# Optimization experiments

Measured on AMD Instinct MI355X. Metric: run time of the kernel, lower is better.

## Reference

```python
import jax, jax.numpy as jnp
import numpy as np

C, CP, H, D, N, B = 128, 16, 8, 16, 2048, 1
INF = 1e8


def _ln(x, w=None, b=None, eps=1e-5):
    mu = jnp.mean(x, axis=-1, keepdims=True)
    var = jnp.var(x, axis=-1, keepdims=True)
    y = (x - mu) * jax.lax.rsqrt(var + eps)
    if w is not None:
        y = y * w
    if b is not None:
        y = y + b
    return y


def _ada_ln(a, s, sln_w, gw, gb, skw):
    # AdaLN: non-affine LN on a, weight-only LN on s, sigmoid gate + skip from s
    a = _ln(a)
    s = _ln(s, sln_w)
    return jax.nn.sigmoid(s @ gw + gb) * a + s @ skw


def _betas(n, n_keys=128, inf=INF):
    # centers at 16 + 32k; query row i belongs to window i//32, keys within +/- n_keys//2 of center
    i = jnp.arange(n)
    c = 16 + 32 * (i // 32)
    j = jnp.arange(n)
    ok = (j[None, :] >= (c - n_keys // 2)[:, None]) & (j[None, :] < (c + n_keys // 2)[:, None])
    return jnp.where(ok, 0.0, -inf).astype(jnp.float32)


def _forward(atom_single, atom_proj, atom_pair, mask,
             a_sln_w, a_gate_w, a_gate_b, a_skip_w,
             wq, bq, wk, wv, wg, bg, wo, bo,
             lnz_w, lnz_b, wz, wog, bog,
             t_sln_w, t_gate_w, t_gate_b, t_skip_w,
             w_sw, w_hid, w_out, t_wog, t_bog):
    bs, n, _ = atom_single.shape
    betas = _betas(n)
    # ---- AttentionPairBias (input_gating=True, residual handled outside) ----
    a = _ada_ln(atom_single, atom_proj, a_sln_w, a_gate_w, a_gate_b, a_skip_w)
    q = (a @ wq + bq).reshape(bs, n, H, D)
    k = (a @ wk).reshape(bs, n, H, D)
    v = (a @ wv).reshape(bs, n, H, D)
    pair_bias = _ln(atom_pair, lnz_w, lnz_b) @ wz            # (bs, n, n, H)
    pair_bias = jnp.transpose(pair_bias, (0, 3, 1, 2)) + betas  # (bs, H, n, n)
    mask_bias = (INF * (mask - 1.0))[:, None, None, :]          # (bs, 1, 1, n)
    logits = jnp.einsum('bqhd,bkhd->bhqk', q, k) / np.float32(np.sqrt(D))
    logits = logits + pair_bias + mask_bias
    probs = jax.nn.softmax(logits, axis=-1)
    o = jnp.einsum('bhqk,bkhd->bqhd', probs, v)
    g = jax.nn.sigmoid(a @ wg + bg).reshape(bs, n, H, D)
    o = (o * g).reshape(bs, n, H * D) @ wo + bo
    o = jax.nn.sigmoid(atom_proj @ wog + bog) * o             # conditioned output gate
    atom_single = atom_single + o
    # ---- ConditionedTransitionBlock (SwiGLU, n=2) ----
    t = _ada_ln(atom_single, atom_proj, t_sln_w, t_gate_w, t_gate_b, t_skip_w)
    hidden = jax.nn.silu(t @ w_sw) * (t @ w_hid)              # (bs, n, 2C)
    t_out = jax.nn.sigmoid(atom_proj @ t_wog + t_bog) * (hidden @ w_out)
    return atom_single + t_out


def setup_inputs() -> dict:
    key = jax.random.key(0)
    ks = iter(jax.random.split(key, 40))
    rn = lambda shape, s=1.0: jax.random.normal(next(ks), shape, jnp.float32) * s
    p = 0.05
    return {
        "atom_single": rn((B, N, C)),
        "atom_proj": rn((B, N, C)),
        "atom_pair": rn((B, N, N, CP)),
        "mask": jnp.ones((B, N), jnp.float32),
        "a_sln_w": jnp.ones((C,), jnp.float32), "a_gate_w": rn((C, C), p), "a_gate_b": jnp.zeros((C,), jnp.float32), "a_skip_w": rn((C, C), p),
        "wq": rn((C, C), p), "bq": jnp.zeros((C,), jnp.float32),
        "wk": rn((C, C), p), "wv": rn((C, C), p),
        "wg": rn((C, C), p), "bg": jnp.ones((C,), jnp.float32),
        "wo": rn((C, C), p), "bo": jnp.zeros((C,), jnp.float32),
        "lnz_w": jnp.ones((CP,), jnp.float32), "lnz_b": jnp.zeros((CP,), jnp.float32), "wz": rn((CP, H), p),
        "wog": rn((C, C), p), "bog": jnp.full((C,), -2.0, jnp.float32),
        "t_sln_w": jnp.ones((C,), jnp.float32), "t_gate_w": rn((C, C), p), "t_gate_b": jnp.zeros((C,), jnp.float32), "t_skip_w": rn((C, C), p),
        "w_sw": rn((C, 2 * C), p), "w_hid": rn((C, 2 * C), p), "w_out": rn((2 * C, C), p),
        "t_wog": rn((C, C), p), "t_bog": jnp.full((C,), -2.0, jnp.float32),
    }


def reference(atom_single, atom_proj, atom_pair, mask,
              a_sln_w, a_gate_w, a_gate_b, a_skip_w,
              wq, bq, wk, wv, wg, bg, wo, bo,
              lnz_w, lnz_b, wz, wog, bog,
              t_sln_w, t_gate_w, t_gate_b, t_skip_w,
              w_sw, w_hid, w_out, t_wog, t_bog):
    out = _forward(atom_single, atom_proj, atom_pair, mask,
                   a_sln_w, a_gate_w, a_gate_b, a_skip_w,
                   wq, bq, wk, wv, wg, bg, wo, bo,
                   lnz_w, lnz_b, wz, wog, bog,
                   t_sln_w, t_gate_w, t_gate_b, t_skip_w,
                   w_sw, w_hid, w_out, t_wog, t_bog)
    return (out, atom_proj, atom_pair)
```

## Files before the change

kernel.cpp:

```cpp
#include <hip/hip_runtime.h>
#include <math.h>

#define NN 2048
#define CC 128
#define HH 8
#define DD 16
#define NKEY 128
#define INFV 1e8f
#define NPR ((long)NN * CC / 4)
#define NCPTOT (NPR + (long)NN * NN * 4)
#define SLOT 2176
#define ANP 36
#define ASLOT 1152

typedef float f4 __attribute__((ext_vector_type(4)));

__device__ __forceinline__ float sigm(float x) { return 1.f / (1.f + expf(-x)); }

struct Args {
  const float *atom_single, *atom_proj, *atom_pair, *mask;
  const float *a_sln_w, *a_gate_w, *a_gate_b, *a_skip_w;
  const float *wq, *bq, *wk, *wv, *wg, *bg, *wo, *bo;
  const float *lnz_w, *lnz_b, *wz, *wog, *bog;
  const float *t_sln_w, *t_gate_w, *t_gate_b, *t_skip_w;
  const float *w_sw, *w_hid, *w_out, *t_wog, *t_bog;
  float *out;
  float *s_ln_t, *a_mat, *qm, *km, *vm, *gm, *ogm, *single2, *t_mat, *hidden, *bias;
  long cut[8];
};

__device__ __forceinline__ void copy_span(const Args& a, int s, long rb, long nb, int tid) {
  long c0 = a.cut[s], c1 = a.cut[s + 1];
  const f4* proj4 = (const f4*)a.atom_proj;
  const f4* pair4 = (const f4*)a.atom_pair;
  f4* dst = (f4*)(a.out + (long)NN * CC);
  long stride = nb * 256;
  long i = c0 + rb * 256 + tid;
  for (; i + 3 * stride < c1; i += 4 * stride) {
    long i1 = i + stride, i2 = i + 2 * stride, i3 = i + 3 * stride;
    f4 x0 = (i  < NPR) ? __builtin_nontemporal_load(&proj4[i])
                       : __builtin_nontemporal_load(&pair4[i - NPR]);
    f4 x1 = (i1 < NPR) ? __builtin_nontemporal_load(&proj4[i1])
                       : __builtin_nontemporal_load(&pair4[i1 - NPR]);
    f4 x2 = (i2 < NPR) ? __builtin_nontemporal_load(&proj4[i2])
                       : __builtin_nontemporal_load(&pair4[i2 - NPR]);
    f4 x3 = (i3 < NPR) ? __builtin_nontemporal_load(&proj4[i3])
                       : __builtin_nontemporal_load(&pair4[i3 - NPR]);
    __builtin_nontemporal_store(x0, &dst[i]);
    __builtin_nontemporal_store(x1, &dst[i1]);
    __builtin_nontemporal_store(x2, &dst[i2]);
    __builtin_nontemporal_store(x3, &dst[i3]);
  }
  for (; i < c1; i += stride) {
    f4 v = (i < NPR) ? __builtin_nontemporal_load(&proj4[i])
                     : __builtin_nontemporal_load(&pair4[i - NPR]);
    __builtin_nontemporal_store(v, &dst[i]);
  }
}

__device__ __forceinline__ void gsingle_pf(float* sm, int tid,
    const float* __restrict__ A1, const float* __restrict__ B1, int lda1, int ldb1, int K1,
    int r0, int c0, float acc1[4][4]) {
  float* buf0 = sm;
  float* buf1 = sm + 2 * SLOT;
  int tr = (tid >> 4) * 4, tc = (tid & 15) * 4;
  int ar = tid >> 5, ak = tid & 31;
  int bk = tid >> 6, bc = tid & 63;
  float pA[2][8], pB[2][8];
  auto LD = [&](int kb, int s) {
#pragma unroll
    for (int j = 0; j < 8; ++j) {
      pA[s][j] = A1[(long)(r0 + ar + 8 * j) * lda1 + kb + ak];
      pB[s][j] = B1[(long)(kb + bk + 4 * j) * ldb1 + c0 + bc];
    }
  };
  auto WR = [&](float* buf, int s) {
    float* B1s_ = buf + SLOT;
#pragma unroll
    for (int j = 0; j < 8; ++j) {
      buf[ak * 68 + ar + 8 * j] = pA[s][j];
      B1s_[(bk + 4 * j) * 68 + bc] = pB[s][j];
    }
  };
  auto CMP = [&](float* cur) {
    float* As_ = cur;
    float* B1s_ = cur + SLOT;
#pragma unroll 4
    for (int k = 0; k < 32; ++k) {
      float4 a1 = *(const float4*)&As_[k * 68 + tr];
      float4 b1 = *(const float4*)&B1s_[k * 68 + tc];
      float a1v[4] = {a1.x, a1.y, a1.z, a1.w};
      float b1v[4] = {b1.x, b1.y, b1.z, b1.w};
#pragma unroll
      for (int i = 0; i < 4; ++i)
#pragma unroll
        for (int j = 0; j < 4; ++j) acc1[i][j] = fmaf(a1v[i], b1v[j], acc1[i][j]);
    }
  };
  int nk = K1 / 32;
  LD(0, 0);
  if (nk > 1) LD(32, 1);
  WR(buf0, 0);
  __syncthreads();
  for (int kt = 0; kt < nk; kt += 2) {
    if (kt + 2 < nk) LD((kt + 2) * 32, 0);
    if (kt + 1 < nk) WR(buf1, 1);
    CMP(buf0);
    __syncthreads();
    if (kt + 1 >= nk) break;
    if (kt + 3 < nk) LD((kt + 3) * 32, 1);
    if (kt + 2 < nk) WR(buf0, 0);
    CMP(buf1);
    __syncthreads();
  }
}

template <bool SHA>
__device__ __forceinline__ void gdual32(float* sm, int tid,
    const float* __restrict__ A1, const float* __restrict__ B1, int lda1, int ldb1, int K1,
    const float* __restrict__ A2, const float* __restrict__ B2, int lda2, int ldb2, int K2,
    int r0, int c0, float acc1[2][4], float acc2[2][4]) {
  const int offB1 = ASLOT;
  const int offA2 = ASLOT + SLOT;
  const int offB2 = SHA ? (ASLOT + SLOT) : (2 * ASLOT + SLOT);
  const int bufsz = SHA ? (ASLOT + 2 * SLOT) : (2 * ASLOT + 2 * SLOT);
  float* buf0 = sm;
  float* buf1 = sm + bufsz;
  int tr2 = (tid >> 4) * 2, tc4 = (tid & 15) * 4;
  int ar = tid & 31, ak4 = (tid >> 5) * 4;
  int bk = tid >> 6, bc = tid & 63;
  float4 vA1[2], vA2[2];
  float pB1[2][8], pB2[2][8];

  auto LD = [&](int kb, int s, bool twof) {
    vA1[s] = *(const float4*)&A1[(long)(r0 + ar) * lda1 + kb + ak4];
#pragma unroll
    for (int j = 0; j < 8; ++j)
      pB1[s][j] = B1[(long)(kb + bk + 4 * j) * ldb1 + c0 + bc];
    if (twof) {
      if constexpr (!SHA) vA2[s] = *(const float4*)&A2[(long)(r0 + ar) * lda2 + kb + ak4];
#pragma unroll
      for (int j = 0; j < 8; ++j)
        pB2[s][j] = B2[(long)(kb + bk + 4 * j) * ldb2 + c0 + bc];
    }
  };
  auto WR = [&](float* buf, int s, bool twof) {
    float* As_ = buf;
    float* B1s_ = buf + offB1;
    As_[(ak4 + 0) * ANP + ar] = vA1[s].x;
    As_[(ak4 + 1) * ANP + ar] = vA1[s].y;
    As_[(ak4 + 2) * ANP + ar] = vA1[s].z;
    As_[(ak4 + 3) * ANP + ar] = vA1[s].w;
#pragma unroll
    for (int j = 0; j < 8; ++j) B1s_[(bk + 4 * j) * 68 + bc] = pB1[s][j];
    if (twof) {
      float* B2s_ = buf + offB2;
      if constexpr (!SHA) {
        float* A2s_ = buf + offA2;
        A2s_[(ak4 + 0) * ANP + ar] = vA2[s].x;
        A2s_[(ak4 + 1) * ANP + ar] = vA2[s].y;
        A2s_[(ak4 + 2) * ANP + ar] = vA2[s].z;
        A2s_[(ak4 + 3) * ANP + ar] = vA2[s].w;
      }
#pragma unroll
      for (int j = 0; j < 8; ++j) B2s_[(bk + 4 * j) * 68 + bc] = pB2[s][j];
    }
  };
  auto CMP = [&](float* cur, bool twoc) {
    float* As_ = cur;
    float* B1s_ = cur + offB1;
    float* A2s_ = cur + offA2;
    float* B2s_ = cur + offB2;
    if (twoc) {
#pragma unroll 4
      for (int k = 0; k < 32; ++k) {
        float2 a1 = *(const float2*)&As_[k * ANP + tr2];
        float4 b1 = *(const float4*)&B1s_[k * 68 + tc4];
        float4 b2 = *(const float4*)&B2s_[k * 68 + tc4];
        float2 a2;
        if constexpr (SHA) a2 = a1; else a2 = *(const float2*)&A2s_[k * ANP + tr2];
        float a1v[2] = {a1.x, a1.y};
        float a2v[2] = {a2.x, a2.y};
        float b1v[4] = {b1.x, b1.y, b1.z, b1.w};
        float b2v[4] = {b2.x, b2.y, b2.z, b2.w};
#pragma unroll
        for (int i = 0; i < 2; ++i)
#pragma unroll
          for (int j = 0; j < 4; ++j) {
            acc1[i][j] = fmaf(a1v[i], b1v[j], acc1[i][j]);
            acc2[i][j] = fmaf(a2v[i], b2v[j], acc2[i][j]);
          }
      }
    } else {
#pragma unroll 4
      for (int k = 0; k < 32; ++k) {
        float2 a1 = *(const float2*)&As_[k * ANP + tr2];
        float4 b1 = *(const float4*)&B1s_[k * 68 + tc4];
        float a1v[2] = {a1.x, a1.y};
        float b1v[4] = {b1.x, b1.y, b1.z, b1.w};
#pragma unroll
        for (int i = 0; i < 2; ++i)
#pragma unroll
          for (int j = 0; j < 4; ++j) acc1[i][j] = fmaf(a1v[i], b1v[j], acc1[i][j]);
      }
    }
  };

  int nk = K1 / 32;
  LD(0, 0, 0 < K2);
  if (nk > 1) LD(32, 1, 32 < K2);
  WR(buf0, 0, 0 < K2);
  __syncthreads();
  for (int kt = 0; kt < nk; kt += 2) {
    if (kt + 2 < nk) LD((kt + 2) * 32, 0, (kt + 2) * 32 < K2);
    if (kt + 1 < nk) WR(buf1, 1, (kt + 1) * 32 < K2);
    CMP(buf0, kt * 32 < K2);
    __syncthreads();
    if (kt + 1 >= nk) break;
    if (kt + 3 < nk) LD((kt + 3) * 32, 1, (kt + 3) * 32 < K2);
    if (kt + 2 < nk) WR(buf0, 0, (kt + 2) * 32 < K2);
    CMP(buf1, (kt + 1) * 32 < K2);
    __syncthreads();
  }
}

__device__ __forceinline__ void gdual32_ln(float* sm, int tid,
    const float* __restrict__ proj, const float* __restrict__ w_ln,
    const float* __restrict__ B1, const float* __restrict__ B2,
    int r0, int c0, const float* sst, float acc1[2][4], float acc2[2][4]) {
  const int offB1 = ASLOT;
  const int offB2 = ASLOT + SLOT;
  const int bufsz = ASLOT + 2 * SLOT;
  float* buf0 = sm;
  float* buf1 = sm + bufsz;
  int tr2 = (tid >> 4) * 2, tc4 = (tid & 15) * 4;
  int ar = tid & 31, ak4 = (tid >> 5) * 4;
  int bk = tid >> 6, bc = tid & 63;
  float4 vA1[2];
  float pB1[2][8], pB2[2][8];

  auto LD = [&](int kb, int s) {
    float4 raw = *(const float4*)&proj[(long)(r0 + ar) * CC + kb + ak4];
    float4 wv = *(const float4*)&w_ln[kb + ak4];
    float mu = sst[2 * ar], rs = sst[2 * ar + 1];
    vA1[s].x = (raw.x - mu) * rs * wv.x;
    vA1[s].y = (raw.y - mu) * rs * wv.y;
    vA1[s].z = (raw.z - mu) * rs * wv.z;
    vA1[s].w = (raw.w - mu) * rs * wv.w;
#pragma unroll
    for (int j = 0; j < 8; ++j) {
      pB1[s][j] = B1[(long)(kb + bk + 4 * j) * CC + c0 + bc];
      pB2[s][j] = B2[(long)(kb + bk + 4 * j) * CC + c0 + bc];
    }
  };
  auto WR = [&](float* buf, int s) {
    float* B1s_ = buf + offB1;
    float* B2s_ = buf + offB2;
    buf[(ak4 + 0) * ANP + ar] = vA1[s].x;
    buf[(ak4 + 1) * ANP + ar] = vA1[s].y;
    buf[(ak4 + 2) * ANP + ar] = vA1[s].z;
    buf[(ak4 + 3) * ANP + ar] = vA1[s].w;
#pragma unroll
    for (int j = 0; j < 8; ++j) {
      B1s_[(bk + 4 * j) * 68 + bc] = pB1[s][j];
      B2s_[(bk + 4 * j) * 68 + bc] = pB2[s][j];
    }
  };
  auto CMP = [&](float* cur) {
    float* As_ = cur;
    float* B1s_ = cur + offB1;
    float* B2s_ = cur + offB2;
#pragma unroll 4
    for (int k = 0; k < 32; ++k) {
      float2 a1 = *(const float2*)&As_[k * ANP + tr2];
      float4 b1 = *(const float4*)&B1s_[k * 68 + tc4];
      float4 b2 = *(const float4*)&B2s_[k * 68 + tc4];
      float a1v[2] = {a1.x, a1.y};
      float b1v[4] = {b1.x, b1.y, b1.z, b1.w};
      float b2v[4] = {b2.x, b2.y, b2.z, b2.w};
#pragma unroll
      for (int i = 0; i < 2; ++i)
#pragma unroll
        for (int j = 0; j < 4; ++j) {
          acc1[i][j] = fmaf(a1v[i], b1v[j], acc1[i][j]);
          acc2[i][j] = fmaf(a1v[i], b2v[j], acc2[i][j]);
        }
    }
  };

  LD(0, 0);
  LD(32, 1);
  WR(buf0, 0);
  __syncthreads();
  LD(64, 0);
  WR(buf1, 1);
  CMP(buf0);
  __syncthreads();
  LD(96, 1);
  WR(buf0, 0);
  CMP(buf1);
  __syncthreads();
  WR(buf1, 1);
  CMP(buf0);
  __syncthreads();
  CMP(buf1);
  __syncthreads();
}

__device__ __forceinline__ void bias_stage(const Args& a, long lo, long hi,
                                           int bid, int nb, int tid, float* sm) {
  float* swz = sm;
  float* swn = sm + 128;
  float* sbn = sm + 144;
  if (tid < 128) swz[tid] = a.wz[tid];
  else if (tid < 144) swn[tid - 128] = a.lnz_w[tid - 128];
  else if (tid < 160) sbn[tid - 144] = a.lnz_b[tid - 144];
  __syncthreads();
  for (long e = lo + bid * 256 + tid; e < hi; e += (long)nb * 256) {
    int q = (int)(e >> 7), kk = (int)(e & 127);
    int k = (q >> 5) * 32 - 48 + kk;
    float o[HH];
    if (k >= 0 && k < NN) {
      const float4* p = (const float4*)(a.atom_pair + ((long)q * NN + k) * 16);
      float4 x0 = p[0], x1 = p[1], x2 = p[2], x3 = p[3];
      float x[16] = {x0.x, x0.y, x0.z, x0.w, x1.x, x1.y, x1.z, x1.w,
                     x2.x, x2.y, x2.z, x2.w, x3.x, x3.y, x3.z, x3.w};
      float s = 0.f, ss = 0.f;
#pragma unroll
      for (int c = 0; c < 16; ++c) { s += x[c]; ss += x[c] * x[c]; }
      float mu = s * (1.f / 16.f);
      float r = rsqrtf(ss * (1.f / 16.f) - mu * mu + 1e-5f);
#pragma unroll
      for (int h = 0; h < HH; ++h) o[h] = 0.f;
#pragma unroll
      for (int c = 0; c < 16; ++c) {
        float y = (x[c] - mu) * r * swn[c] + sbn[c];
#pragma unroll
        for (int h = 0; h < HH; ++h) o[h] = fmaf(y, swz[c * HH + h], o[h]);
      }
      float mb = INFV * (a.mask[k] - 1.f);
#pragma unroll
      for (int h = 0; h < HH; ++h) o[h] += mb;
    } else {
#pragma unroll
      for (int h = 0; h < HH; ++h) o[h] = -INFV;
    }
#pragma unroll
    for (int h = 0; h < HH; ++h) a.bias[(long)h * NN * NKEY + e] = o[h];
  }
}

__device__ __forceinline__ void adaln_a_ln(const Args& a, int bid, int tid,
                                           float* sm, float* sst) {
  int r0 = (bid & 63) * 32, c0 = (bid >> 6) * 64;
  {
    int row = tid >> 3, cg = (tid & 7) * 16;
    const float* sp = a.atom_proj + (long)(r0 + row) * CC + cg;
    const float* ss_ = a.atom_single + (long)(r0 + row) * CC + cg;
    float s1 = 0.f, q1 = 0.f, s2 = 0.f, q2 = 0.f;
#pragma unroll
    for (int j = 0; j < 4; ++j) {
      float4 v = *(const float4*)(sp + j * 4);
      s1 += v.x + v.y + v.z + v.w;
      q1 += v.x * v.x + v.y * v.y + v.z * v.z + v.w * v.w;
      float4 u = *(const float4*)(ss_ + j * 4);
      s2 += u.x + u.y + u.z + u.w;
      q2 += u.x * u.x + u.y * u.y + u.z * u.z + u.w * u.w;
    }
#pragma unroll
    for (int m = 1; m < 8; m <<= 1) {
      s1 += __shfl_xor(s1, m); q1 += __shfl_xor(q1, m);
      s2 += __shfl_xor(s2, m); q2 += __shfl_xor(q2, m);
    }
    if ((tid & 7) == 0) {
      float mu1 = s1 * (1.f / CC);
      sst[2 * row] = mu1;
      sst[2 * row + 1] = rsqrtf(q1 * (1.f / CC) - mu1 * mu1 + 1e-5f);
      float mu2 = s2 * (1.f / CC);
      sst[64 + 2 * row] = mu2;
      sst[64 + 2 * row + 1] = rsqrtf(q2 * (1.f / CC) - mu2 * mu2 + 1e-5f);
    }
  }
  __syncthreads();
  float acc1[2][4] = {{0}}, acc2[2][4] = {{0}};
  gdual32_ln(sm, tid, a.atom_proj, a.a_sln_w, a.a_gate_w, a.a_skip_w,
             r0, c0, sst, acc1, acc2);
  int tr2 = (tid >> 4) * 2, tc4 = (tid & 15) * 4;
#pragma unroll
  for (int i = 0; i < 2; ++i) {
    long r = r0 + tr2 + i;
    float mup = sst[2 * (tr2 + i)], rsp = sst[2 * (tr2 + i) + 1];
    float mus = sst[64 + 2 * (tr2 + i)], rss = sst[64 + 2 * (tr2 + i) + 1];
    float4 sv = *(const float4*)(a.atom_single + r * CC + c0 + tc4);
    float4 pv = *(const float4*)(a.atom_proj + r * CC + c0 + tc4);
    float4 wt = *(const float4*)(a.t_sln_w + c0 + tc4);
    float lnm[4] = {(sv.x - mus) * rss, (sv.y - mus) * rss,
                    (sv.z - mus) * rss, (sv.w - mus) * rss};
    float lnp[4] = {(pv.x - mup) * rsp, (pv.y - mup) * rsp,
                    (pv.z - mup) * rsp, (pv.w - mup) * rsp};
    float wtv[4] = {wt.x, wt.y, wt.z, wt.w};
    float o[4];
#pragma unroll
    for (int j = 0; j < 4; ++j)
      o[j] = sigm(acc1[i][j] + a.a_gate_b[c0 + tc4 + j]) * lnm[j] + acc2[i][j];
    *(float4*)(a.a_mat + r * CC + c0 + tc4) = make_float4(o[0], o[1], o[2], o[3]);
    *(float4*)(a.s_ln_t + r * CC + c0 + tc4) =
        make_float4(lnp[0] * wtv[0], lnp[1] * wtv[1], lnp[2] * wtv[2], lnp[3] * wtv[3]);
  }
}

template <bool INLN>
__device__ __forceinline__ void adaln32_stage(const Args& a, const float* A, const float* gw,
                                              const float* gb, const float* skw,
                                              const float* lnm_or_src, float* outp,
                                              int bid, int tid, float* sm, float* sst) {
  int r0 = (bid & 63) * 32, c0 = (bid >> 6) * 64;
  if constexpr (INLN) {
    int row = tid >> 3, cg = (tid & 7) * 16;
    const float* src = lnm_or_src + (long)(r0 + row) * CC + cg;
    float s = 0.f, ss = 0.f;
#pragma unroll
    for (int j = 0; j < 4; ++j) {
      float4 v = *(const float4*)(src + j * 4);
      s += v.x + v.y + v.z + v.w;
      ss += v.x * v.x + v.y * v.y + v.z * v.z + v.w * v.w;
    }
#pragma unroll
    for (int m = 1; m < 8; m <<= 1) { s += __shfl_xor(s, m); ss += __shfl_xor(ss, m); }
    if ((tid & 7) == 0) {
      float mu = s * (1.f / CC);
      sst[2 * row] = mu;
      sst[2 * row + 1] = rsqrtf(ss * (1.f / CC) - mu * mu + 1e-5f);
    }
  }
  float acc1[2][4] = {{0}}, acc2[2][4] = {{0}};
  gdual32<true>(sm, tid, A, gw, 128, 128, 128, A, skw, 128, 128, 128, r0, c0, acc1, acc2);
  int tr2 = (tid >> 4) * 2, tc4 = (tid & 15) * 4;
#pragma unroll
  for (int i = 0; i < 2; ++i) {
    long r = r0 + tr2 + i;
    float lv[4];
    if constexpr (INLN) {
      float mu = sst[2 * (tr2 + i)], rr = sst[2 * (tr2 + i) + 1];
      float4 sv = *(const float4*)(lnm_or_src + r * CC + c0 + tc4);
      lv[0] = (sv.x - mu) * rr; lv[1] = (sv.y - mu) * rr;
      lv[2] = (sv.z - mu) * rr; lv[3] = (sv.w - mu) * rr;
    } else {
      float4 lm = *(const float4*)(lnm_or_src + r * CC + c0 + tc4);
      lv[0] = lm.x; lv[1] = lm.y; lv[2] = lm.z; lv[3] = lm.w;
    }
    float o[4];
#pragma unroll
    for (int j = 0; j < 4; ++j)
      o[j] = sigm(acc1[i][j] + gb[c0 + tc4 + j]) * lv[j] + acc2[i][j];
    *(float4*)(outp + r * CC + c0 + tc4) = make_float4(o[0], o[1], o[2], o[3]);
  }
}

__device__ __forceinline__ void gemm4_stage(const Args& a, int bid, int tid, float* sm) {
  int r0 = (bid & 31) * 64;
  int cg4 = (bid >> 5) * 64;
  int mat = cg4 >> 7;
  int c0 = cg4 & 127;
  const float* B = (mat == 0) ? a.wq : (mat == 1) ? a.wk : (mat == 2) ? a.wv : a.wg;
  float acc[4][4] = {{0}};
  gsingle_pf(sm, tid, a.a_mat, B, 128, 128, 128, r0, c0, acc);
  float* outp = (mat == 0) ? a.qm : (mat == 1) ? a.km : (mat == 2) ? a.vm : a.gm;
  int tr = (tid >> 4) * 4, tc = (tid & 15) * 4;
#pragma unroll
  for (int i = 0; i < 4; ++i) {
    long r = r0 + tr + i;
    float o[4];
#pragma unroll
    for (int j = 0; j < 4; ++j) {
      float x = acc[i][j];
      if (mat == 0) x += a.bq[c0 + tc + j];
      if (mat == 3) x = sigm(x + a.bg[c0 + tc + j]);
      o[j] = x;
    }
    *(float4*)(outp + r * CC + c0 + tc) = make_float4(o[0], o[1], o[2], o[3]);
  }
}

__device__ __forceinline__ void attn_unit(const Args& a, int u, int tid, float* sm) {
  int w = u & 63, h = u >> 6;
  int q0 = w * 32, k0 = w * 32 - 48;
  float* Qs = sm;
  float* Ks = sm + 544;
  float* Vs = sm + 3104;
  float* Ps = sm + 5664;
  for (int i = tid; i < 32 * 16; i += 256) {
    int qi = i >> 4, d = i & 15;
    Qs[qi * 17 + d] = a.qm[(long)(q0 + qi) * CC + h * DD + d];
  }
  for (int i = tid; i < 128 * 16; i += 256) {
    int kk = i >> 4, d = i & 15;
    int k = k0 + kk;
    bool ok = (k >= 0 && k < NN);
    Ks[kk * 20 + d] = ok ? a.km[(long)k * CC + h * DD + d] : 0.f;
    Vs[kk * 20 + d] = ok ? a.vm[(long)k * CC + h * DD + d] : 0.f;
  }
  __syncthreads();
  int qi = tid >> 3, kg = tid & 7;
  const float* brow = a.bias + (long)h * NN * NKEY + (long)(q0 + qi) * NKEY;
  float qreg[16];
#pragma unroll
  for (int d = 0; d < 16; ++d) qreg[d] = Qs[qi * 17 + d];
  float l[16];
#pragma unroll
  for (int j = 0; j < 16; ++j) {
    int kk = kg + 8 * j;
    const float4* kr = (const float4*)&Ks[kk * 20];
    float4 k0v = kr[0], k1v = kr[1], k2v = kr[2], k3v = kr[3];
    float acc = 0.f;
    acc = fmaf(qreg[0], k0v.x, acc);  acc = fmaf(qreg[1], k0v.y, acc);
    acc = fmaf(qreg[2], k0v.z, acc);  acc = fmaf(qreg[3], k0v.w, acc);
    acc = fmaf(qreg[4], k1v.x, acc);  acc = fmaf(qreg[5], k1v.y, acc);
    acc = fmaf(qreg[6], k1v.z, acc);  acc = fmaf(qreg[7], k1v.w, acc);
    acc = fmaf(qreg[8], k2v.x, acc);  acc = fmaf(qreg[9], k2v.y, acc);
    acc = fmaf(qreg[10], k2v.z, acc); acc = fmaf(qreg[11], k2v.w, acc);
    acc = fmaf(qreg[12], k3v.x, acc); acc = fmaf(qreg[13], k3v.y, acc);
    acc = fmaf(qreg[14], k3v.z, acc); acc = fmaf(qreg[15], k3v.w, acc);
    l[j] = acc * 0.25f + brow[kk];
  }
  float m = l[0];
#pragma unroll
  for (int j = 1; j < 16; ++j) m = fmaxf(m, l[j]);
#pragma unroll
  for (int mm = 1; mm < 8; mm <<= 1) m = fmaxf(m, __shfl_xor(m, mm));
  float sum = 0.f;
#pragma unroll
  for (int j = 0; j < 16; ++j) { l[j] = expf(l[j] - m); sum += l[j]; }
#pragma unroll
  for (int mm = 1; mm < 8; mm <<= 1) sum += __shfl_xor(sum, mm);
  float inv = 1.f / sum;
#pragma unroll
  for (int j = 0; j < 16; ++j) Ps[qi * 132 + kg + 8 * j] = l[j] * inv;
  __syncthreads();
  int d0 = tid & 7;
  float o0 = 0.f, o1 = 0.f;
#pragma unroll 8
  for (int kk = 0; kk < 128; ++kk) {
    float p = Ps[qi * 132 + kk];
    o0 = fmaf(p, Vs[kk * 20 + d0], o0);
    o1 = fmaf(p, Vs[kk * 20 + d0 + 8], o1);
  }
  long base = (long)(q0 + qi) * CC + h * DD;
  a.ogm[base + d0] = o0 * a.gm[base + d0];
  a.ogm[base + d0 + 8] = o1 * a.gm[base + d0 + 8];
}

__device__ __forceinline__ void out1_32(const Args& a, int bid, int tid, float* sm) {
  int r0 = (bid & 63) * 32, c0 = (bid >> 6) * 64;
  float accX[2][4] = {{0}}, accW[2][4] = {{0}};
  gdual32<false>(sm, tid, a.ogm, a.wo, 128, 128, 128, a.atom_proj, a.wog, 128, 128, 128,
                 r0, c0, accX, accW);
  int tr2 = (tid >> 4) * 2, tc4 = (tid & 15) * 4;
#pragma unroll
  for (int i = 0; i < 2; ++i) {
    long r = r0 + tr2 + i;
    float4 sv = *(const float4*)(a.atom_single + r * CC + c0 + tc4);
    float s[4] = {sv.x, sv.y, sv.z, sv.w};
    float o[4];
#pragma unroll
    for (int j = 0; j < 4; ++j) {
      int c = c0 + tc4 + j;
      o[j] = s[j] + sigm(accW[i][j] + a.bog[c]) * (accX[i][j] + a.bo[c]);
    }
    *(float4*)(a.single2 + r * CC + c0 + tc4) = make_float4(o[0], o[1], o[2], o[3]);
  }
}

__device__ __forceinline__ void swiglu_32(const Args& a, int bid, int tid, float* sm) {
  int r0 = (bid & 63) * 32, c0 = (bid >> 6) * 64;
  float acc1[2][4] = {{0}}, acc2[2][4] = {{0}};
  gdual32<true>(sm, tid, a.t_mat, a.w_sw, 128, 256, 128, a.t_mat, a.w_hid, 128, 256, 128,
                r0, c0, acc1, acc2);
  int tr2 = (tid >> 4) * 2, tc4 = (tid & 15) * 4;
#pragma unroll
  for (int i = 0; i < 2; ++i) {
    long r = r0 + tr2 + i;
    float o[4];
#pragma unroll
    for (int j = 0; j < 4; ++j) {
      float x = acc1[i][j];
      o[j] = x * sigm(x) * acc2[i][j];
    }
    *(float4*)(a.hidden + r * 256 + c0 + tc4) = make_float4(o[0], o[1], o[2], o[3]);
  }
}

__device__ __forceinline__ void out2_32(const Args& a, int bid, int tid, float* sm) {
  int r0 = (bid & 63) * 32, c0 = (bid >> 6) * 64;
  float accX[2][4] = {{0}}, accW[2][4] = {{0}};
  gdual32<false>(sm, tid, a.hidden, a.w_out, 256, 128, 256, a.atom_proj, a.t_wog, 128, 128, 128,
                 r0, c0, accX, accW);
  int tr2 = (tid >> 4) * 2, tc4 = (tid & 15) * 4;
#pragma unroll
  for (int i = 0; i < 2; ++i) {
    long r = r0 + tr2 + i;
    float4 sv = *(const float4*)(a.single2 + r * CC + c0 + tc4);
    float s[4] = {sv.x, sv.y, sv.z, sv.w};
    float o[4];
#pragma unroll
    for (int j = 0; j < 4; ++j) {
      int c = c0 + tc4 + j;
      o[j] = s[j] + sigm(accW[i][j] + a.t_bog[c]) * accX[i][j];
    }
    *(float4*)(a.out + r * CC + c0 + tc4) = make_float4(o[0], o[1], o[2], o[3]);
  }
}

#define BIAS_TOT ((long)NN * NKEY)
#define BIAS_H (BIAS_TOT / 2)

__global__ __launch_bounds__(256) void k_adaln_a(Args a) {
  __shared__ __align__(16) float sm[2 * (ASLOT + 2 * SLOT) + 128];
  int bid = blockIdx.x, tid = threadIdx.x;
  if (bid < 128) adaln_a_ln(a, bid, tid, sm, sm + 2 * (ASLOT + 2 * SLOT));
  else if (bid < 256) bias_stage(a, 0, BIAS_H, bid - 128, 128, tid, sm);
  else copy_span(a, 0, bid - 256, gridDim.x - 256, tid);
}

__global__ __launch_bounds__(256) void k_qkvg(Args a) {
  __shared__ __align__(16) float sm[2 * 2 * SLOT];
  int bid = blockIdx.x, tid = threadIdx.x;
  if (bid < 256) gemm4_stage(a, bid, tid, sm);
  else if (bid < 384) bias_stage(a, BIAS_H, BIAS_TOT, bid - 256, 128, tid, sm);
  else copy_span(a, 1, bid - 384, gridDim.x - 384, tid);
}

__global__ __launch_bounds__(256) void k_attn(Args a) {
  __shared__ __align__(16) float sm[9888];
  int bid = blockIdx.x, tid = threadIdx.x;
  if (bid < 512) attn_unit(a, bid, tid, sm);
  else copy_span(a, 2, bid - 512, gridDim.x - 512, tid);
}

__global__ __launch_bounds__(256) void k_out1(Args a) {
  __shared__ __align__(16) float sm[2 * (2 * ASLOT + 2 * SLOT)];
  int bid = blockIdx.x, tid = threadIdx.x;
  if (bid < 128) out1_32(a, bid, tid, sm);
  else copy_span(a, 3, bid - 128, gridDim.x - 128, tid);
}

__global__ __launch_bounds__(256) void k_adaln_t(Args a) {
  __shared__ __align__(16) float sm[2 * (ASLOT + 2 * SLOT) + 64];
  int bid = blockIdx.x, tid = threadIdx.x;
  if (bid < 128)
    adaln32_stage<true>(a, a.s_ln_t, a.t_gate_w, a.t_gate_b, a.t_skip_w, a.single2, a.t_mat,
                        bid, tid, sm, sm + 2 * (ASLOT + 2 * SLOT));
  else copy_span(a, 4, bid - 128, gridDim.x - 128, tid);
}

__global__ __launch_bounds__(256) void k_swiglu(Args a) {
  __shared__ __align__(16) float sm[2 * (ASLOT + 2 * SLOT)];
  int bid = blockIdx.x, tid = threadIdx.x;
  if (bid < 256) swiglu_32(a, bid, tid, sm);
  else copy_span(a, 5, bid - 256, gridDim.x - 256, tid);
}

__global__ __launch_bounds__(256) void k_out2(Args a) {
  __shared__ __align__(16) float sm[2 * (2 * ASLOT + 2 * SLOT)];
  int bid = blockIdx.x, tid = threadIdx.x;
  if (bid < 128) out2_32(a, bid, tid, sm);
  else copy_span(a, 6, bid - 128, gridDim.x - 128, tid);
}

extern "C" void kernel_launch(void* const* d_in, const int* in_sizes, int n_in,
                              void* d_out, int out_size, void* d_ws, size_t ws_size,
                              hipStream_t stream) {
  (void)in_sizes; (void)n_in; (void)out_size; (void)ws_size;
  Args a;
  a.atom_single = (const float*)d_in[0];
  a.atom_proj   = (const float*)d_in[1];
  a.atom_pair   = (const float*)d_in[2];
  a.mask        = (const float*)d_in[3];
  a.a_sln_w  = (const float*)d_in[4];
  a.a_gate_w = (const float*)d_in[5];
  a.a_gate_b = (const float*)d_in[6];
  a.a_skip_w = (const float*)d_in[7];
  a.wq = (const float*)d_in[8];  a.bq = (const float*)d_in[9];
  a.wk = (const float*)d_in[10]; a.wv = (const float*)d_in[11];
  a.wg = (const float*)d_in[12]; a.bg = (const float*)d_in[13];
  a.wo = (const float*)d_in[14]; a.bo = (const float*)d_in[15];
  a.lnz_w = (const float*)d_in[16]; a.lnz_b = (const float*)d_in[17];
  a.wz = (const float*)d_in[18];
  a.wog = (const float*)d_in[19]; a.bog = (const float*)d_in[20];
  a.t_sln_w  = (const float*)d_in[21];
  a.t_gate_w = (const float*)d_in[22];
  a.t_gate_b = (const float*)d_in[23];
  a.t_skip_w = (const float*)d_in[24];
  a.w_sw  = (const float*)d_in[25];
  a.w_hid = (const float*)d_in[26];
  a.w_out = (const float*)d_in[27];
  a.t_wog = (const float*)d_in[28];
  a.t_bog = (const float*)d_in[29];
  a.out = (float*)d_out;

  float* ws = (float*)d_ws;
  const long NC = (long)NN * CC;
  a.s_ln_t  = ws + 0 * NC;
  a.a_mat   = ws + 1 * NC;
  a.qm      = ws + 2 * NC;
  a.km      = ws + 3 * NC;
  a.vm      = ws + 4 * NC;
  a.gm      = ws + 5 * NC;
  a.ogm     = ws + 6 * NC;
  a.single2 = ws + 7 * NC;
  a.t_mat   = ws + 8 * NC;
  a.hidden  = ws + 9 * NC;
  a.bias    = ws + 11 * NC;

  const int cum[8] = {0, 11, 23, 37, 44, 51, 58, 64};
  for (int i = 0; i < 8; ++i) a.cut[i] = NCPTOT * (long)cum[i] / 64;

  k_adaln_a<<<2048, 256, 0, stream>>>(a);
  k_qkvg   <<<2048, 256, 0, stream>>>(a);
  k_attn   <<<2048, 256, 0, stream>>>(a);
  k_out1   <<<2048, 256, 0, stream>>>(a);
  k_adaln_t<<<2048, 256, 0, stream>>>(a);
  k_swiglu <<<2048, 256, 0, stream>>>(a);
  k_out2   <<<2048, 256, 0, stream>>>(a);
}
```

Before: 136.8 us.

## Store intermediate workspace tensors and attention bias in bf16

Converts most intermediate workspace buffers (LN outputs, q/k/v/g, gated attention output, transition hidden, pair bias) from fp32 to bf16 storage. Values are rounded on store and widened back to fp32 on load, so the math stays fp32. The aim is to halve the bytes moved through memory between stages. Rounding the intermediates to bf16 costs accuracy, and the bias values of -1e8 lose precision.

```diff
diff --git a/kernel.cpp b/kernel.cpp
--- a/kernel.cpp
+++ b/kernel.cpp
@@ -14,8 +14,17 @@
 #define ASLOT 1152
 
 typedef float f4 __attribute__((ext_vector_type(4)));
+typedef unsigned short bf16;
 
 __device__ __forceinline__ float sigm(float x) { return 1.f / (1.f + expf(-x)); }
+__device__ __forceinline__ bf16 f2b(float x) {
+  unsigned u = __float_as_uint(x);
+  u += 0x7FFF + ((u >> 16) & 1);
+  return (bf16)(u >> 16);
+}
+__device__ __forceinline__ float b2f(bf16 b) {
+  return __uint_as_float(((unsigned)b) << 16);
+}
 
 struct Args {
   const float *atom_single, *atom_proj, *atom_pair, *mask;
@@ -25,7 +34,8 @@
   const float *t_sln_w, *t_gate_w, *t_gate_b, *t_skip_w;
   const float *w_sw, *w_hid, *w_out, *t_wog, *t_bog;
   float *out;
-  float *s_ln_t, *a_mat, *qm, *km, *vm, *gm, *ogm, *single2, *t_mat, *hidden, *bias;
+  bf16 *s_ln_t, *a_mat, *qm, *km, *vm, *gm, *ogm, *t_mat, *hidden, *bias;
+  float *single2;
   long cut[8];
 };
 
@@ -59,7 +69,7 @@
 }
 
 __device__ __forceinline__ void gsingle_pf(float* sm, int tid,
-    const float* __restrict__ A1, const float* __restrict__ B1, int lda1, int ldb1, int K1,
+    const bf16* __restrict__ A1, const float* __restrict__ B1, int lda1, int ldb1, int K1,
     int r0, int c0, float acc1[4][4]) {
   float* buf0 = sm;
   float* buf1 = sm + 2 * SLOT;
@@ -70,7 +80,7 @@
   auto LD = [&](int kb, int s) {
 #pragma unroll
     for (int j = 0; j < 8; ++j) {
-      pA[s][j] = A1[(long)(r0 + ar + 8 * j) * lda1 + kb + ak];
+      pA[s][j] = b2f(A1[(long)(r0 + ar + 8 * j) * lda1 + kb + ak]);
       pB[s][j] = B1[(long)(kb + bk + 4 * j) * ldb1 + c0 + bc];
     }
   };
@@ -115,15 +125,17 @@
   }
 }
 
-template <bool SHA>
+template <bool SHA, bool BF1>
 __device__ __forceinline__ void gdual32(float* sm, int tid,
-    const float* __restrict__ A1, const float* __restrict__ B1, int lda1, int ldb1, int K1,
+    const void* A1v, const float* __restrict__ B1, int lda1, int ldb1, int K1,
     const float* __restrict__ A2, const float* __restrict__ B2, int lda2, int ldb2, int K2,
     int r0, int c0, float acc1[2][4], float acc2[2][4]) {
   const int offB1 = ASLOT;
   const int offA2 = ASLOT + SLOT;
   const int offB2 = SHA ? (ASLOT + SLOT) : (2 * ASLOT + SLOT);
   const int bufsz = SHA ? (ASLOT + 2 * SLOT) : (2 * ASLOT + 2 * SLOT);
+  const float* A1f = (const float*)A1v;
+  const bf16* A1b = (const bf16*)A1v;
   float* buf0 = sm;
   float* buf1 = sm + bufsz;
   int tr2 = (tid >> 4) * 2, tc4 = (tid & 15) * 4;
@@ -133,7 +145,12 @@
   float pB1[2][8], pB2[2][8];
 
   auto LD = [&](int kb, int s, bool twof) {
-    vA1[s] = *(const float4*)&A1[(long)(r0 + ar) * lda1 + kb + ak4];
+    if constexpr (BF1) {
+      ushort4 rw = *(const ushort4*)&A1b[(long)(r0 + ar) * lda1 + kb + ak4];
+      vA1[s] = make_float4(b2f(rw.x), b2f(rw.y), b2f(rw.z), b2f(rw.w));
+    } else {
+      vA1[s] = *(const float4*)&A1f[(long)(r0 + ar) * lda1 + kb + ak4];
+    }
 #pragma unroll
     for (int j = 0; j < 8; ++j)
       pB1[s][j] = B1[(long)(kb + bk + 4 * j) * ldb1 + c0 + bc];
@@ -346,7 +363,7 @@
       for (int h = 0; h < HH; ++h) o[h] = -INFV;
     }
 #pragma unroll
-    for (int h = 0; h < HH; ++h) a.bias[(long)h * NN * NKEY + e] = o[h];
+    for (int h = 0; h < HH; ++h) a.bias[(long)h * NN * NKEY + e] = f2b(o[h]);
   }
 }
 
@@ -403,21 +420,20 @@
 #pragma unroll
     for (int j = 0; j < 4; ++j)
       o[j] = sigm(acc1[i][j] + a.a_gate_b[c0 + tc4 + j]) * lnm[j] + acc2[i][j];
-    *(float4*)(a.a_mat + r * CC + c0 + tc4) = make_float4(o[0], o[1], o[2], o[3]);
-    *(float4*)(a.s_ln_t + r * CC + c0 + tc4) =
-        make_float4(lnp[0] * wtv[0], lnp[1] * wtv[1], lnp[2] * wtv[2], lnp[3] * wtv[3]);
-  }
-}
-
-template <bool INLN>
-__device__ __forceinline__ void adaln32_stage(const Args& a, const float* A, const float* gw,
-                                              const float* gb, const float* skw,
-                                              const float* lnm_or_src, float* outp,
-                                              int bid, int tid, float* sm, float* sst) {
+    *(ushort4*)(a.a_mat + r * CC + c0 + tc4) =
+        make_ushort4(f2b(o[0]), f2b(o[1]), f2b(o[2]), f2b(o[3]));
+    *(ushort4*)(a.s_ln_t + r * CC + c0 + tc4) =
+        make_ushort4(f2b(lnp[0] * wtv[0]), f2b(lnp[1] * wtv[1]),
+                     f2b(lnp[2] * wtv[2]), f2b(lnp[3] * wtv[3]));
+  }
+}
+
+__device__ __forceinline__ void adaln_t_stage(const Args& a, int bid, int tid,
+                                              float* sm, float* sst) {
   int r0 = (bid & 63) * 32, c0 = (bid >> 6) * 64;
-  if constexpr (INLN) {
+  {
     int row = tid >> 3, cg = (tid & 7) * 16;
-    const float* src = lnm_or_src + (long)(r0 + row) * CC + cg;
+    const float* src = a.single2 + (long)(r0 + row) * CC + cg;
     float s = 0.f, ss = 0.f;
 #pragma unroll
     for (int j = 0; j < 4; ++j) {
@@ -434,26 +450,21 @@
     }
   }
   float acc1[2][4] = {{0}}, acc2[2][4] = {{0}};
-  gdual32<true>(sm, tid, A, gw, 128, 128, 128, A, skw, 128, 128, 128, r0, c0, acc1, acc2);
+  gdual32<true, true>(sm, tid, a.s_ln_t, a.t_gate_w, 128, 128, 128,
+                      nullptr, a.t_skip_w, 128, 128, 128, r0, c0, acc1, acc2);
   int tr2 = (tid >> 4) * 2, tc4 = (tid & 15) * 4;
 #pragma unroll
   for (int i = 0; i < 2; ++i) {
     long r = r0 + tr2 + i;
-    float lv[4];
-    if constexpr (INLN) {
-      float mu = sst[2 * (tr2 + i)], rr = sst[2 * (tr2 + i) + 1];
-      float4 sv = *(const float4*)(lnm_or_src + r * CC + c0 + tc4);
-      lv[0] = (sv.x - mu) * rr; lv[1] = (sv.y - mu) * rr;
-      lv[2] = (sv.z - mu) * rr; lv[3] = (sv.w - mu) * rr;
-    } else {
-      float4 lm = *(const float4*)(lnm_or_src + r * CC + c0 + tc4);
-      lv[0] = lm.x; lv[1] = lm.y; lv[2] = lm.z; lv[3] = lm.w;
-    }
+    float mu = sst[2 * (tr2 + i)], rr = sst[2 * (tr2 + i) + 1];
+    float4 sv = *(const float4*)(a.single2 + r * CC + c0 + tc4);
+    float lv[4] = {(sv.x - mu) * rr, (sv.y - mu) * rr, (sv.z - mu) * rr, (sv.w - mu) * rr};
     float o[4];
 #pragma unroll
     for (int j = 0; j < 4; ++j)
-      o[j] = sigm(acc1[i][j] + gb[c0 + tc4 + j]) * lv[j] + acc2[i][j];
-    *(float4*)(outp + r * CC + c0 + tc4) = make_float4(o[0], o[1], o[2], o[3]);
+      o[j] = sigm(acc1[i][j] + a.t_gate_b[c0 + tc4 + j]) * lv[j] + acc2[i][j];
+    *(ushort4*)(a.t_mat + r * CC + c0 + tc4) =
+        make_ushort4(f2b(o[0]), f2b(o[1]), f2b(o[2]), f2b(o[3]));
   }
 }
 
@@ -465,7 +476,7 @@
   const float* B = (mat == 0) ? a.wq : (mat == 1) ? a.wk : (mat == 2) ? a.wv : a.wg;
   float acc[4][4] = {{0}};
   gsingle_pf(sm, tid, a.a_mat, B, 128, 128, 128, r0, c0, acc);
-  float* outp = (mat == 0) ? a.qm : (mat == 1) ? a.km : (mat == 2) ? a.vm : a.gm;
+  bf16* outp = (mat == 0) ? a.qm : (mat == 1) ? a.km : (mat == 2) ? a.vm : a.gm;
   int tr = (tid >> 4) * 4, tc = (tid & 15) * 4;
 #pragma unroll
   for (int i = 0; i < 4; ++i) {
@@ -478,7 +489,8 @@
       if (mat == 3) x = sigm(x + a.bg[c0 + tc + j]);
       o[j] = x;
     }
-    *(float4*)(outp + r * CC + c0 + tc) = make_float4(o[0], o[1], o[2], o[3]);
+    *(ushort4*)(outp + r * CC + c0 + tc) =
+        make_ushort4(f2b(o[0]), f2b(o[1]), f2b(o[2]), f2b(o[3]));
   }
 }
 
@@ -491,18 +503,18 @@
   float* Ps = sm + 5664;
   for (int i = tid; i < 32 * 16; i += 256) {
     int qi = i >> 4, d = i & 15;
-    Qs[qi * 17 + d] = a.qm[(long)(q0 + qi) * CC + h * DD + d];
+    Qs[qi * 17 + d] = b2f(a.qm[(long)(q0 + qi) * CC + h * DD + d]);
   }
   for (int i = tid; i < 128 * 16; i += 256) {
     int kk = i >> 4, d = i & 15;
     int k = k0 + kk;
     bool ok = (k >= 0 && k < NN);
-    Ks[kk * 20 + d] = ok ? a.km[(long)k * CC + h * DD + d] : 0.f;
-    Vs[kk * 20 + d] = ok ? a.vm[(long)k * CC + h * DD + d] : 0.f;
+    Ks[kk * 20 + d] = ok ? b2f(a.km[(long)k * CC + h * DD + d]) : 0.f;
+    Vs[kk * 20 + d] = ok ? b2f(a.vm[(long)k * CC + h * DD + d]) : 0.f;
   }
   __syncthreads();
   int qi = tid >> 3, kg = tid & 7;
-  const float* brow = a.bias + (long)h * NN * NKEY + (long)(q0 + qi) * NKEY;
+  const bf16* brow = a.bias + (long)h * NN * NKEY + (long)(q0 + qi) * NKEY;
   float qreg[16];
 #pragma unroll
   for (int d = 0; d < 16; ++d) qreg[d] = Qs[qi * 17 + d];
@@ -521,7 +533,7 @@
     acc = fmaf(qreg[10], k2v.z, acc); acc = fmaf(qreg[11], k2v.w, acc);
     acc = fmaf(qreg[12], k3v.x, acc); acc = fmaf(qreg[13], k3v.y, acc);
     acc = fmaf(qreg[14], k3v.z, acc); acc = fmaf(qreg[15], k3v.w, acc);
-    l[j] = acc * 0.25f + brow[kk];
+    l[j] = acc * 0.25f + b2f(brow[kk]);
   }
   float m = l[0];
 #pragma unroll
@@ -546,15 +558,15 @@
     o1 = fmaf(p, Vs[kk * 20 + d0 + 8], o1);
   }
   long base = (long)(q0 + qi) * CC + h * DD;
-  a.ogm[base + d0] = o0 * a.gm[base + d0];
-  a.ogm[base + d0 + 8] = o1 * a.gm[base + d0 + 8];
+  a.ogm[base + d0] = f2b(o0 * b2f(a.gm[base + d0]));
+  a.ogm[base + d0 + 8] = f2b(o1 * b2f(a.gm[base + d0 + 8]));
 }
 
 __device__ __forceinline__ void out1_32(const Args& a, int bid, int tid, float* sm) {
   int r0 = (bid & 63) * 32, c0 = (bid >> 6) * 64;
   float accX[2][4] = {{0}}, accW[2][4] = {{0}};
-  gdual32<false>(sm, tid, a.ogm, a.wo, 128, 128, 128, a.atom_proj, a.wog, 128, 128, 128,
-                 r0, c0, accX, accW);
+  gdual32<false, true>(sm, tid, a.ogm, a.wo, 128, 128, 128,
+                       a.atom_proj, a.wog, 128, 128, 128, r0, c0, accX, accW);
   int tr2 = (tid >> 4) * 2, tc4 = (tid & 15) * 4;
 #pragma unroll
   for (int i = 0; i < 2; ++i) {
@@ -574,8 +586,8 @@
 __device__ __forceinline__ void swiglu_32(const Args& a, int bid, int tid, float* sm) {
   int r0 = (bid & 63) * 32, c0 = (bid >> 6) * 64;
   float acc1[2][4] = {{0}}, acc2[2][4] = {{0}};
-  gdual32<true>(sm, tid, a.t_mat, a.w_sw, 128, 256, 128, a.t_mat, a.w_hid, 128, 256, 128,
-                r0, c0, acc1, acc2);
+  gdual32<true, true>(sm, tid, a.t_mat, a.w_sw, 128, 256, 128,
+                      nullptr, a.w_hid, 128, 256, 128, r0, c0, acc1, acc2);
   int tr2 = (tid >> 4) * 2, tc4 = (tid & 15) * 4;
 #pragma unroll
   for (int i = 0; i < 2; ++i) {
@@ -586,15 +598,16 @@
       float x = acc1[i][j];
       o[j] = x * sigm(x) * acc2[i][j];
     }
-    *(float4*)(a.hidden + r * 256 + c0 + tc4) = make_float4(o[0], o[1], o[2], o[3]);
+    *(ushort4*)(a.hidden + r * 256 + c0 + tc4) =
+        make_ushort4(f2b(o[0]), f2b(o[1]), f2b(o[2]), f2b(o[3]));
   }
 }
 
 __device__ __forceinline__ void out2_32(const Args& a, int bid, int tid, float* sm) {
   int r0 = (bid & 63) * 32, c0 = (bid >> 6) * 64;
   float accX[2][4] = {{0}}, accW[2][4] = {{0}};
-  gdual32<false>(sm, tid, a.hidden, a.w_out, 256, 128, 256, a.atom_proj, a.t_wog, 128, 128, 128,
-                 r0, c0, accX, accW);
+  gdual32<false, true>(sm, tid, a.hidden, a.w_out, 256, 128, 256,
+                       a.atom_proj, a.t_wog, 128, 128, 128, r0, c0, accX, accW);
   int tr2 = (tid >> 4) * 2, tc4 = (tid & 15) * 4;
 #pragma unroll
   for (int i = 0; i < 2; ++i) {
@@ -647,9 +660,7 @@
 __global__ __launch_bounds__(256) void k_adaln_t(Args a) {
   __shared__ __align__(16) float sm[2 * (ASLOT + 2 * SLOT) + 64];
   int bid = blockIdx.x, tid = threadIdx.x;
-  if (bid < 128)
-    adaln32_stage<true>(a, a.s_ln_t, a.t_gate_w, a.t_gate_b, a.t_skip_w, a.single2, a.t_mat,
-                        bid, tid, sm, sm + 2 * (ASLOT + 2 * SLOT));
+  if (bid < 128) adaln_t_stage(a, bid, tid, sm, sm + 2 * (ASLOT + 2 * SLOT));
   else copy_span(a, 4, bid - 128, gridDim.x - 128, tid);
 }
 
@@ -700,17 +711,17 @@
 
   float* ws = (float*)d_ws;
   const long NC = (long)NN * CC;
-  a.s_ln_t  = ws + 0 * NC;
-  a.a_mat   = ws + 1 * NC;
-  a.qm      = ws + 2 * NC;
-  a.km      = ws + 3 * NC;
-  a.vm      = ws + 4 * NC;
-  a.gm      = ws + 5 * NC;
-  a.ogm     = ws + 6 * NC;
+  a.s_ln_t  = (bf16*)(ws + 0 * NC);
+  a.a_mat   = (bf16*)(ws + 1 * NC);
+  a.qm      = (bf16*)(ws + 2 * NC);
+  a.km      = (bf16*)(ws + 3 * NC);
+  a.vm      = (bf16*)(ws + 4 * NC);
+  a.gm      = (bf16*)(ws + 5 * NC);
+  a.ogm     = (bf16*)(ws + 6 * NC);
   a.single2 = ws + 7 * NC;
-  a.t_mat   = ws + 8 * NC;
-  a.hidden  = ws + 9 * NC;
-  a.bias    = ws + 11 * NC;
+  a.t_mat   = (bf16*)(ws + 9 * NC);
+  a.hidden  = (bf16*)(ws + 10 * NC);
+  a.bias    = (bf16*)(ws + 12 * NC);
 
   const int cum[8] = {0, 11, 23, 37, 44, 51, 58, 64};
   for (int i = 0; i < 8; ++i) a.cut[i] = NCPTOT * (long)cum[i] / 64;
```

Result: no change. 134.6 us (-1.7%).
